# Kernel optimization log

Measured on AMD Instinct MI355X. Metric: run time of the kernel, lower is better.

## Reference

```python
import jax, jax.numpy as jnp
import numpy as np

N, E = 50000, 800000
IN_DIM, HID, OUT = 128, 64, 64
NEG_SLOPE = 0.2  # PyG GATConv default leaky_relu slope


def glorot(key, shape):
    fan_in, fan_out = shape[0], shape[-1]
    lim = jnp.sqrt(6.0 / (fan_in + fan_out))
    return jax.random.uniform(key, shape, minval=-lim, maxval=lim, dtype=jnp.float32)


def setup_inputs() -> dict:
    key = jax.random.key(0)
    ks = jax.random.split(key, 10)
    x = jax.random.normal(ks[0], (N, IN_DIM), dtype=jnp.float32)
    edge_index = jax.random.randint(ks[1], (2, E), 0, N, dtype=jnp.int64)
    # GATConv layer 1: heads=2, concat=False
    W1 = glorot(ks[2], (IN_DIM, 2 * HID))
    att_src1 = glorot(ks[3], (1, 2, HID))[0]   # [2, HID]
    att_dst1 = glorot(ks[4], (1, 2, HID))[0]
    b1 = jnp.zeros((HID,), jnp.float32)
    # GATConv layer 2: heads=1, concat=False
    W2 = glorot(ks[5], (HID, OUT))
    att_src2 = glorot(ks[6], (1, 1, OUT))[0]   # [1, OUT]
    att_dst2 = glorot(ks[7], (1, 1, OUT))[0]
    b2 = jnp.zeros((OUT,), jnp.float32)
    return {"x": x, "edge_index": edge_index, "W1": W1, "att_src1": att_src1,
            "att_dst1": att_dst1, "b1": b1, "W2": W2, "att_src2": att_src2,
            "att_dst2": att_dst2, "b2": b2}


def gat_conv(x, src, dst, W, att_src, att_dst, bias, heads, out_ch):
    n = x.shape[0]
    h = (x @ W).reshape(n, heads, out_ch)              # [N,H,C]
    a_src = jnp.einsum('nhc,hc->nh', h, att_src)       # [N,H]
    a_dst = jnp.einsum('nhc,hc->nh', h, att_dst)
    e = jax.nn.leaky_relu(a_src[src] + a_dst[dst], NEG_SLOPE)  # [E,H]
    # softmax over incoming edges per destination node (stable)
    e_max = jax.ops.segment_max(e, dst, num_segments=n)
    ex = jnp.exp(e - e_max[dst])
    denom = jax.ops.segment_sum(ex, dst, num_segments=n)
    alpha = ex / (denom[dst] + 1e-16)                  # [E,H]
    msg = h[src] * alpha[:, :, None]                   # [E,H,C]
    out = jax.ops.segment_sum(msg, dst, num_segments=n)
    return out.mean(axis=1) + bias                     # concat=False -> head mean


def reference(x, edge_index, W1, att_src1, att_dst1, b1, W2, att_src2, att_dst2, b2):
    n = x.shape[0]
    loop = jnp.arange(n, dtype=edge_index.dtype)
    src = jnp.concatenate([edge_index[0], loop])       # PyG add_self_loops
    dst = jnp.concatenate([edge_index[1], loop])
    x1 = gat_conv(x, src, dst, W1, att_src1, att_dst1, b1, 2, HID)
    x1 = jax.nn.elu(x1)
    # eval mode: dropedge and dropout are identity
    out = gat_conv(x1, src, dst, W2, att_src2, att_dst2, b2, 1, OUT)
    return out
```

## Files before the change

### kernel.cpp

```cpp
#include <hip/hip_runtime.h>
#include <math.h>

#define IN_DIM 128
#define HID 64
#define NEG_SLOPE 0.2f
#define CHUNK 4096
#define GCAP 6144

typedef __attribute__((ext_vector_type(8))) short bf16x8;
typedef __attribute__((ext_vector_type(4))) float f32x4;
typedef __attribute__((ext_vector_type(2))) float v2f;

__device__ __forceinline__ float wmax(float v){
  #pragma unroll
  for (int o = 32; o > 0; o >>= 1) v = fmaxf(v, __shfl_xor(v, o));
  return v;
}
__device__ __forceinline__ float wsum(float v){
  #pragma unroll
  for (int o = 32; o > 0; o >>= 1) v += __shfl_xor(v, o);
  return v;
}
__device__ __forceinline__ unsigned short f2bf(float f){
  union { float f; unsigned u; } v; v.f = f;
  unsigned r = v.u + 0x7fffu + ((v.u >> 16) & 1u);
  return (unsigned short)(r >> 16);
}
__device__ __forceinline__ float bl(unsigned u){
  union { unsigned u; float f; } v; v.u = u << 16; return v.f;
}
__device__ __forceinline__ float bh(unsigned u){
  union { unsigned u; float f; } v; v.u = u & 0xffff0000u; return v.f;
}
__device__ __forceinline__ v2f up2(unsigned u){
  v2f r; r[0] = bl(u); r[1] = bh(u); return r;
}

__device__ __forceinline__ void incl_scan256(int* sh, int tid){
  #pragma unroll
  for (int off = 1; off < 256; off <<= 1){
    int v = sh[tid];
    if (tid >= off) v += sh[tid - off];
    __syncthreads();
    sh[tid] = v;
    __syncthreads();
  }
}


__global__ __launch_bounds__(256) void pack_hist(const int* __restrict__ ei, int E,
                                                 unsigned* __restrict__ packed,
                                                 int* __restrict__ binCnt){
  __shared__ int lh[256];
  int tid = threadIdx.x;
  lh[tid] = 0; __syncthreads();
  int base = blockIdx.x * CHUNK;
  #pragma unroll
  for (int j = 0; j < CHUNK / 256; j++){
    int e = base + j * 256 + tid;
    if (e < E){
      unsigned s = (unsigned)ei[e];
      unsigned d = (unsigned)ei[E + e];
      unsigned pk = (d << 16) | s;
      packed[e] = pk;
      atomicAdd(&lh[d >> 8], 1);
    }
  }
  __syncthreads();
  if (lh[tid] > 0) atomicAdd(&binCnt[tid], lh[tid]);
}

__global__ __launch_bounds__(256) void scan_bins(const int* __restrict__ binCnt,
                                                 int* __restrict__ binBase,
                                                 int* __restrict__ binCursor,
                                                 int* __restrict__ row_ptr,
                                                 int NG, int N, int E){
  __shared__ int sh[256];
  int tid = threadIdx.x;
  sh[tid] = (tid < NG) ? binCnt[tid] : 0;
  __syncthreads();
  incl_scan256(sh, tid);
  int excl = tid ? sh[tid - 1] : 0;
  if (tid < NG){ binBase[tid] = excl; binCursor[tid] = excl; }
  if (tid == 0) row_ptr[N] = E;
}

__global__ __launch_bounds__(256) void scatter_bins(const unsigned* __restrict__ packed, int E,
                                                    int* __restrict__ binCursor,
                                                    unsigned* __restrict__ binned){
  __shared__ int lh[256], lbase[256], gpos[256], lcur[256];
  __shared__ unsigned buf[CHUNK];
  int tid = threadIdx.x;
  lh[tid] = 0; __syncthreads();
  int base = blockIdx.x * CHUNK;
  int rem = E - base;
  unsigned v[CHUNK / 256];
  #pragma unroll
  for (int j = 0; j < CHUNK / 256; j++){
    int i = j * 256 + tid;
    if (i < rem){ v[j] = packed[base + i]; atomicAdd(&lh[v[j] >> 24], 1); }
  }
  __syncthreads();
  lbase[tid] = lh[tid]; __syncthreads();
  incl_scan256(lbase, tid);
  int myExcl = tid ? lbase[tid - 1] : 0;
  __syncthreads();
  lbase[tid] = myExcl;
  lcur[tid] = myExcl;
  if (lh[tid] > 0) gpos[tid] = atomicAdd(&binCursor[tid], lh[tid]);
  __syncthreads();
  #pragma unroll
  for (int j = 0; j < CHUNK / 256; j++){
    int i = j * 256 + tid;
    if (i < rem){
      int b = v[j] >> 24;
      int p = atomicAdd(&lcur[b], 1);
      buf[p] = v[j];
    }
  }
  __syncthreads();
  int cn = rem < CHUNK ? rem : CHUNK;
  for (int i = tid; i < cn; i += 256){
    unsigned u = buf[i];
    int b = u >> 24;
    binned[gpos[b] + (i - lbase[b])] = u;
  }
}

__global__ __launch_bounds__(256) void group_sort(const unsigned* __restrict__ binned,
                                                  const int* __restrict__ binBase,
                                                  const int* __restrict__ binCnt,
                                                  unsigned* __restrict__ sorted,
                                                  int* __restrict__ row_ptr, int N){
  __shared__ unsigned A[GCAP], B[GCAP];
  __shared__ int h2[256], rs[256], cur[256];
  int g = blockIdx.x, tid = threadIdx.x;
  int base = binBase[g];
  int cnt = binCnt[g]; if (cnt > GCAP) cnt = GCAP;
  h2[tid] = 0; __syncthreads();
  for (int i = tid; i < cnt; i += 256){
    unsigned u = binned[base + i];
    A[i] = u;
    atomicAdd(&h2[(u >> 16) & 255], 1);
  }
  __syncthreads();
  rs[tid] = h2[tid]; __syncthreads();
  incl_scan256(rs, tid);
  int excl = tid ? rs[tid - 1] : 0;
  __syncthreads();
  rs[tid] = excl; cur[tid] = excl;
  int d = g * 256 + tid;
  if (d < N) row_ptr[d] = base + excl;
  __syncthreads();
  for (int i = tid; i < cnt; i += 256){
    unsigned u = A[i];
    int p = atomicAdd(&cur[(u >> 16) & 255], 1);
    B[p] = u;
  }
  __syncthreads();
  for (int i = tid; i < cnt; i += 256)
    sorted[base + i] = B[i];
}


__global__ void convert_w(const float* __restrict__ W1, const float* __restrict__ W2,
                          unsigned short* __restrict__ W1t, unsigned short* __restrict__ W2t){
  int tid = blockIdx.x * 256 + threadIdx.x;
  if (tid < 128 * 128){
    int n = tid >> 7, k = tid & 127;
    W1t[n * 128 + k] = f2bf(W1[k * 128 + n]);
  }
  int t2 = tid - 128 * 128;
  if (t2 >= 0 && t2 < 64 * 64){
    int n = t2 >> 6, k = t2 & 63;
    W2t[n * 64 + k] = f2bf(W2[k * 64 + n]);
  }
}

template<int K, int NC, int HEADS>
__global__ __launch_bounds__(512) void gemm_mfma(const float* __restrict__ X,
    const unsigned short* __restrict__ Wt, const float* __restrict__ asrc,
    const float* __restrict__ adst, unsigned short* __restrict__ Hb,
    float* __restrict__ aa, int n_rows)
{
  constexpr int MT = 128;
  constexpr int KP = K + 8;
  constexpr int CP = NC + 4;
  constexpr int MF = MT / 16;
  constexpr int NFt = NC / 16;
  constexpr int WPN = 8 / NFt;
  constexpr int MFW = MF / WPN;
  constexpr unsigned SM1 = (unsigned)(MT + NC) * KP * 2;
  constexpr unsigned SM2 = (unsigned)MT * CP * 4;
  __shared__ char smem[SM1 > SM2 ? SM1 : SM2];
  unsigned short* xa = (unsigned short*)smem;
  unsigned short* wl = xa + MT * KP;
  int tid = threadIdx.x;
  int n0 = blockIdx.x * MT;

  for (int idx = tid; idx < MT * (K / 4); idx += 512){
    int n = idx / (K / 4), k4 = idx % (K / 4);
    float4 v = make_float4(0.f, 0.f, 0.f, 0.f);
    if (n0 + n < n_rows) v = *(const float4*)&X[(size_t)(n0 + n) * K + k4 * 4];
    ushort4 pk; pk.x = f2bf(v.x); pk.y = f2bf(v.y); pk.z = f2bf(v.z); pk.w = f2bf(v.w);
    *(ushort4*)&xa[n * KP + k4 * 4] = pk;
  }
  for (int idx = tid; idx < NC * (K / 8); idx += 512){
    int n = idx / (K / 8), k8 = idx % (K / 8);
    uint4 v = *(const uint4*)&Wt[(size_t)n * K + k8 * 8];
    *(uint4*)&wl[n * KP + k8 * 8] = v;
  }
  __syncthreads();

  int lane = tid & 63, w = tid >> 6;
  int m = lane & 15, q = lane >> 4;
  int nf = w % NFt;
  int mseg = w / NFt;
  f32x4 acc[MFW];
  #pragma unroll
  for (int i = 0; i < MFW; i++)
    #pragma unroll
    for (int r = 0; r < 4; r++) acc[i][r] = 0.f;

  #pragma unroll
  for (int ks = 0; ks < K / 32; ks++){
    bf16x8 bg = *(const bf16x8*)&wl[(nf * 16 + m) * KP + ks * 32 + q * 8];
    #pragma unroll
    for (int i = 0; i < MFW; i++){
      bf16x8 af = *(const bf16x8*)&xa[((mseg * MFW + i) * 16 + m) * KP + ks * 32 + q * 8];
      acc[i] = __builtin_amdgcn_mfma_f32_16x16x32_bf16(af, bg, acc[i], 0, 0, 0);
    }
  }
  __syncthreads();
  float* C = (float*)smem;
  #pragma unroll
  for (int i = 0; i < MFW; i++)
    #pragma unroll
    for (int r = 0; r < 4; r++)
      C[((mseg * MFW + i) * 16 + q * 4 + r) * CP + nf * 16 + m] = acc[i][r];
  __syncthreads();

  constexpr int CH = NC / 4;
  int row = tid >> 2;
  int c0 = (tid & 3) * CH;
  int n = n0 + row;
  int head = (HEADS == 2) ? (c0 >> 6) : 0;
  float s_p = 0.f, d_p = 0.f;
  unsigned short hb[CH];
  #pragma unroll
  for (int c = 0; c < CH; c += 4){
    f32x4 v = *(const f32x4*)&C[row * CP + c0 + c];
    #pragma unroll
    for (int u = 0; u < 4; u++){
      int ch = (c0 + c + u) & 63;
      s_p += v[u] * asrc[head * 64 + ch];
      d_p += v[u] * adst[head * 64 + ch];
      hb[c + u] = f2bf(v[u]);
    }
  }
  if (n < n_rows){
    #pragma unroll
    for (int c = 0; c < CH; c += 8){
      uint4 pk;
      pk.x = (unsigned)hb[c]     | ((unsigned)hb[c + 1] << 16);
      pk.y = (unsigned)hb[c + 2] | ((unsigned)hb[c + 3] << 16);
      pk.z = (unsigned)hb[c + 4] | ((unsigned)hb[c + 5] << 16);
      pk.w = (unsigned)hb[c + 6] | ((unsigned)hb[c + 7] << 16);
      *(uint4*)&Hb[(size_t)n * NC + c0 + c] = pk;
    }
  }
  s_p += __shfl_xor(s_p, 1);
  d_p += __shfl_xor(d_p, 1);
  if (HEADS == 2){
    if ((tid & 1) == 0 && n < n_rows){
      aa[(size_t)n * 4 + head]     = s_p;
      aa[(size_t)n * 4 + 2 + head] = d_p;
    }
  } else {
    s_p += __shfl_xor(s_p, 2);
    d_p += __shfl_xor(d_p, 2);
    if ((tid & 3) == 0 && n < n_rows){
      aa[(size_t)n * 2]     = s_p;
      aa[(size_t)n * 2 + 1] = d_p;
    }
  }
}


__global__ void agg_layer1(const int* __restrict__ row_ptr, const unsigned* __restrict__ sorted,
                           const float* __restrict__ aa, const unsigned short* __restrict__ h1b,
                           const float* __restrict__ b1, float* __restrict__ x1, int n_nodes){
  int d = (blockIdx.x * blockDim.x + threadIdx.x) >> 6;
  int lane = threadIdx.x & 63;
  if (d >= n_nodes) return;
  int rp0 = row_ptr[d];
  int deg = row_ptr[d + 1] - rp0;
  float2 adv = *(const float2*)&aa[d * 4 + 2];
  int s = -1;
  if (lane < deg) s = (int)(sorted[rp0 + lane] & 0xffffu);
  else if (lane == deg) s = d;
  float e0 = -INFINITY, e1 = -INFINITY;
  if (s >= 0){
    float2 asv = *(const float2*)&aa[s * 4];
    float t0 = asv.x + adv.x;
    float t1 = asv.y + adv.y;
    e0 = t0 >= 0.f ? t0 : NEG_SLOPE * t0;
    e1 = t1 >= 0.f ? t1 : NEG_SLOPE * t1;
  }
  float m0 = wmax(e0), m1 = wmax(e1);
  float p0 = (s >= 0) ? __expf(e0 - m0) : 0.f;
  float p1 = (s >= 0) ? __expf(e1 - m1) : 0.f;
  float al0 = p0 / (wsum(p0) + 1e-16f);
  float al1 = p1 / (wsum(p1) + 1e-16f);
  int ne = deg + 1;
  int g = lane >> 4, c = lane & 15;
  v2f acc[4] = {{0.f,0.f},{0.f,0.f},{0.f,0.f},{0.f,0.f}};
  #pragma unroll 2
  for (int j0 = 0; j0 < ne; j0 += 4){
    int j = j0 + g;
    int sj = __shfl(s, j);
    float a0 = __shfl(al0, j);
    float a1 = __shfl(al1, j);
    if (j < ne){
      uint4 v = ((const uint4*)(h1b + (size_t)sj * 128))[c];
      float a = (c < 8) ? a0 : a1;
      v2f av = {a, a};
      acc[0] = av * up2(v.x) + acc[0];
      acc[1] = av * up2(v.y) + acc[1];
      acc[2] = av * up2(v.z) + acc[2];
      acc[3] = av * up2(v.w) + acc[3];
    }
  }
  float accf[8] = {acc[0][0], acc[0][1], acc[1][0], acc[1][1],
                   acc[2][0], acc[2][1], acc[3][0], acc[3][1]};
  #pragma unroll
  for (int i = 0; i < 8; i++){
    accf[i] += __shfl_xor(accf[i], 16);
    accf[i] += __shfl_xor(accf[i], 32);
  }
  float outv[8];
  #pragma unroll
  for (int i = 0; i < 8; i++){
    float o = __shfl_xor(accf[i], 8);
    outv[i] = 0.5f * (accf[i] + o);
  }
  if (g == 0 && c < 8){
    float r[8];
    #pragma unroll
    for (int i = 0; i < 8; i++){
      float v = outv[i] + b1[c * 8 + i];
      r[i] = v > 0.f ? v : expm1f(v);
    }
    float* p = &x1[(size_t)d * 64 + c * 8];
    *(float4*)p       = make_float4(r[0], r[1], r[2], r[3]);
    *(float4*)(p + 4) = make_float4(r[4], r[5], r[6], r[7]);
  }
}

__global__ void agg_layer2(const int* __restrict__ row_ptr, const unsigned* __restrict__ sorted,
                           const float* __restrict__ aa, const unsigned short* __restrict__ h2b,
                           const float* __restrict__ b2, float* __restrict__ out, int n_nodes){
  int d = (blockIdx.x * blockDim.x + threadIdx.x) >> 6;
  int lane = threadIdx.x & 63;
  if (d >= n_nodes) return;
  int rp0 = row_ptr[d];
  int deg = row_ptr[d + 1] - rp0;
  float ad = aa[d * 2 + 1];
  int s = -1;
  if (lane < deg) s = (int)(sorted[rp0 + lane] & 0xffffu);
  else if (lane == deg) s = d;
  float e = -INFINITY;
  if (s >= 0){
    float t = aa[s * 2 + 0] + ad;
    e = t >= 0.f ? t : NEG_SLOPE * t;
  }
  float m = wmax(e);
  float p = (s >= 0) ? __expf(e - m) : 0.f;
  float al = p / (wsum(p) + 1e-16f);
  int ne = deg + 1;
  int g = lane >> 3, c = lane & 7;
  v2f acc[4] = {{0.f,0.f},{0.f,0.f},{0.f,0.f},{0.f,0.f}};
  #pragma unroll 2
  for (int j0 = 0; j0 < ne; j0 += 8){
    int j = j0 + g;
    int sj = __shfl(s, j);
    float a = __shfl(al, j);
    if (j < ne){
      uint4 v = ((const uint4*)(h2b + (size_t)sj * 64))[c];
      v2f av = {a, a};
      acc[0] = av * up2(v.x) + acc[0];
      acc[1] = av * up2(v.y) + acc[1];
      acc[2] = av * up2(v.z) + acc[2];
      acc[3] = av * up2(v.w) + acc[3];
    }
  }
  float accf[8] = {acc[0][0], acc[0][1], acc[1][0], acc[1][1],
                   acc[2][0], acc[2][1], acc[3][0], acc[3][1]};
  #pragma unroll
  for (int i = 0; i < 8; i++){
    accf[i] += __shfl_xor(accf[i], 8);
    accf[i] += __shfl_xor(accf[i], 16);
    accf[i] += __shfl_xor(accf[i], 32);
  }
  if (lane < 8){
    float r[8];
    #pragma unroll
    for (int i = 0; i < 8; i++) r[i] = accf[i] + b2[lane * 8 + i];
    float* q = &out[(size_t)d * 64 + lane * 8];
    *(float4*)q       = make_float4(r[0], r[1], r[2], r[3]);
    *(float4*)(q + 4) = make_float4(r[4], r[5], r[6], r[7]);
  }
}

extern "C" void kernel_launch(void* const* d_in, const int* in_sizes, int n_in,
                              void* d_out, int out_size, void* d_ws, size_t ws_size,
                              hipStream_t stream){
  const float* x     = (const float*)d_in[0];
  const int*   ei    = (const int*)d_in[1];
  const float* W1    = (const float*)d_in[2];
  const float* asrc1 = (const float*)d_in[3];
  const float* adst1 = (const float*)d_in[4];
  const float* b1    = (const float*)d_in[5];
  const float* W2    = (const float*)d_in[6];
  const float* asrc2 = (const float*)d_in[7];
  const float* adst2 = (const float*)d_in[8];
  const float* b2    = (const float*)d_in[9];
  float* out = (float*)d_out;
  int N = in_sizes[0] / IN_DIM;
  int E = in_sizes[1] / 2;
  int NG = (N + 255) >> 8;
  int NBLK = (E + CHUNK - 1) / CHUNK;

  char* p = (char*)d_ws;
  unsigned short* h1b = (unsigned short*)p;  p += (size_t)N * 128 * 2;
  unsigned short* h2b = (unsigned short*)p;  p += (size_t)N * 64 * 2;
  float* x1  = (float*)p;                    p += (size_t)N * 64 * 4;
  float* aa1 = (float*)p;                    p += (size_t)N * 4 * 4;
  float* aa2 = (float*)p;                    p += (size_t)N * 2 * 4;
  unsigned* packed = (unsigned*)p;           p += (size_t)E * 4;
  unsigned* binned = (unsigned*)p;           p += (size_t)E * 4;
  unsigned* sorted = (unsigned*)p;           p += (size_t)E * 4;
  int* row_ptr   = (int*)p;                  p += (size_t)(N + 1) * 4;
  int* binCnt    = (int*)p;                  p += 256 * 4;
  int* binBase   = (int*)p;                  p += 256 * 4;
  int* binCursor = (int*)p;                  p += 256 * 4;
  unsigned short* W1t = (unsigned short*)p;  p += 128 * 128 * 2;
  unsigned short* W2t = (unsigned short*)p;

  hipMemsetAsync(binCnt, 0, 256 * sizeof(int), stream);
  convert_w<<<(128 * 128 + 64 * 64 + 255) / 256, 256, 0, stream>>>(W1, W2, W1t, W2t);
  pack_hist<<<NBLK, 256, 0, stream>>>(ei, E, packed, binCnt);
  scan_bins<<<1, 256, 0, stream>>>(binCnt, binBase, binCursor, row_ptr, NG, N, E);
  scatter_bins<<<NBLK, 256, 0, stream>>>(packed, E, binCursor, binned);
  group_sort<<<NG, 256, 0, stream>>>(binned, binBase, binCnt, sorted, row_ptr, N);
  gemm_mfma<128, 128, 2><<<(N + 127) / 128, 512, 0, stream>>>(
      x, W1t, asrc1, adst1, h1b, aa1, N);
  agg_layer1<<<(N + 3) / 4, 256, 0, stream>>>(row_ptr, sorted, aa1, h1b, b1, x1, N);
  gemm_mfma<64, 64, 1><<<(N + 127) / 128, 512, 0, stream>>>(
      x1, W2t, asrc2, adst2, h2b, aa2, N);
  agg_layer2<<<(N + 3) / 4, 256, 0, stream>>>(row_ptr, sorted, aa2, h2b, b2, out, N);
}
```

Baseline: 237.3 us.

## Slice hidden features per XCD and precompute attention weights before aggregation

The GEMM epilogue now writes the bf16 hidden features in a channel-sliced layout: four 16-word slices for layer 1 and two for layer 2. Attention softmax coefficients are computed in separate kernels and stored per edge, reusing dead workspace buffers. The aggregation kernels interleave block indices so that each XCD in the round-robin dispatch always gathers the same feature slice. This is meant to let each slice's gather working set fit in a per-XCD L2. The cost is narrower 4-byte gathers, with edge indices and alphas re-read once per slice, plus two extra launches.

```diff
diff --git a/kernel.cpp b/kernel.cpp
--- a/kernel.cpp
+++ b/kernel.cpp
@@ -180,8 +180,8 @@
 template<int K, int NC, int HEADS>
 __global__ __launch_bounds__(512) void gemm_mfma(const float* __restrict__ X,
     const unsigned short* __restrict__ Wt, const float* __restrict__ asrc,
-    const float* __restrict__ adst, unsigned short* __restrict__ Hb,
-    float* __restrict__ aa, int n_rows)
+    const float* __restrict__ adst, unsigned* __restrict__ Hs,
+    float* __restrict__ aa, int n_rows, int Nn)
 {
   constexpr int MT = 128;
   constexpr int KP = K + 8;
@@ -240,56 +240,65 @@
       C[((mseg * MFW + i) * 16 + q * 4 + r) * CP + nf * 16 + m] = acc[i][r];
   __syncthreads();
 
-  constexpr int CH = NC / 4;
   int row = tid >> 2;
-  int c0 = (tid & 3) * CH;
   int n = n0 + row;
-  int head = (HEADS == 2) ? (c0 >> 6) : 0;
-  float s_p = 0.f, d_p = 0.f;
-  unsigned short hb[CH];
-  #pragma unroll
-  for (int c = 0; c < CH; c += 4){
-    f32x4 v = *(const f32x4*)&C[row * CP + c0 + c];
+  if (HEADS == 2){
+    int sl = tid & 3;
+    float s0 = 0.f, s1 = 0.f, d0 = 0.f, d1 = 0.f;
+    unsigned pk[16];
     #pragma unroll
-    for (int u = 0; u < 4; u++){
-      int ch = (c0 + c + u) & 63;
-      s_p += v[u] * asrc[head * 64 + ch];
-      d_p += v[u] * adst[head * 64 + ch];
-      hb[c + u] = f2bf(v[u]);
-    }
-  }
-  if (n < n_rows){
+    for (int c = 0; c < 16; c++){
+      int ch = sl * 16 + c;
+      float v0 = C[row * CP + ch];
+      float v1 = C[row * CP + 64 + ch];
+      s0 += v0 * asrc[ch];      d0 += v0 * adst[ch];
+      s1 += v1 * asrc[64 + ch]; d1 += v1 * adst[64 + ch];
+      pk[c] = (unsigned)f2bf(v0) | ((unsigned)f2bf(v1) << 16);
+    }
+    if (n < n_rows){
+      uint4* dst = (uint4*)&Hs[((size_t)sl * Nn + n) * 16];
+      #pragma unroll
+      for (int q4 = 0; q4 < 4; q4++)
+        dst[q4] = make_uint4(pk[q4*4], pk[q4*4+1], pk[q4*4+2], pk[q4*4+3]);
+    }
+    s0 += __shfl_xor(s0, 1); s1 += __shfl_xor(s1, 1);
+    d0 += __shfl_xor(d0, 1); d1 += __shfl_xor(d1, 1);
+    s0 += __shfl_xor(s0, 2); s1 += __shfl_xor(s1, 2);
+    d0 += __shfl_xor(d0, 2); d1 += __shfl_xor(d1, 2);
+    if (sl == 0 && n < n_rows)
+      *(float4*)&aa[(size_t)n * 4] = make_float4(s0, s1, d0, d1);
+  } else {
+    int qt = tid & 3;
+    int sl = qt >> 1, half = qt & 1;
+    float sp = 0.f, dp = 0.f;
+    unsigned pk[8];
     #pragma unroll
-    for (int c = 0; c < CH; c += 8){
-      uint4 pk;
-      pk.x = (unsigned)hb[c]     | ((unsigned)hb[c + 1] << 16);
-      pk.y = (unsigned)hb[c + 2] | ((unsigned)hb[c + 3] << 16);
-      pk.z = (unsigned)hb[c + 4] | ((unsigned)hb[c + 5] << 16);
-      pk.w = (unsigned)hb[c + 6] | ((unsigned)hb[c + 7] << 16);
-      *(uint4*)&Hb[(size_t)n * NC + c0 + c] = pk;
-    }
-  }
-  s_p += __shfl_xor(s_p, 1);
-  d_p += __shfl_xor(d_p, 1);
-  if (HEADS == 2){
-    if ((tid & 1) == 0 && n < n_rows){
-      aa[(size_t)n * 4 + head]     = s_p;
-      aa[(size_t)n * 4 + 2 + head] = d_p;
-    }
-  } else {
-    s_p += __shfl_xor(s_p, 2);
-    d_p += __shfl_xor(d_p, 2);
-    if ((tid & 3) == 0 && n < n_rows){
-      aa[(size_t)n * 2]     = s_p;
-      aa[(size_t)n * 2 + 1] = d_p;
-    }
-  }
-}
-
-
-__global__ void agg_layer1(const int* __restrict__ row_ptr, const unsigned* __restrict__ sorted,
-                           const float* __restrict__ aa, const unsigned short* __restrict__ h1b,
-                           const float* __restrict__ b1, float* __restrict__ x1, int n_nodes){
+    for (int c2 = 0; c2 < 8; c2++){
+      int ch = qt * 16 + c2 * 2;
+      float v0 = C[row * CP + ch];
+      float v1 = C[row * CP + ch + 1];
+      sp += v0 * asrc[ch] + v1 * asrc[ch + 1];
+      dp += v0 * adst[ch] + v1 * adst[ch + 1];
+      pk[c2] = (unsigned)f2bf(v0) | ((unsigned)f2bf(v1) << 16);
+    }
+    if (n < n_rows){
+      uint4* dst = (uint4*)&Hs[((size_t)sl * Nn + n) * 16 + half * 8];
+      dst[0] = make_uint4(pk[0], pk[1], pk[2], pk[3]);
+      dst[1] = make_uint4(pk[4], pk[5], pk[6], pk[7]);
+    }
+    sp += __shfl_xor(sp, 1); dp += __shfl_xor(dp, 1);
+    sp += __shfl_xor(sp, 2); dp += __shfl_xor(dp, 2);
+    if (qt == 0 && n < n_rows){
+      aa[(size_t)n * 2]     = sp;
+      aa[(size_t)n * 2 + 1] = dp;
+    }
+  }
+}
+
+
+__global__ void alpha1_k(const int* __restrict__ row_ptr, const unsigned* __restrict__ sorted,
+                         const float* __restrict__ aa, float2* __restrict__ alpha,
+                         float2* __restrict__ aself, int n_nodes){
   int d = (blockIdx.x * blockDim.x + threadIdx.x) >> 6;
   int lane = threadIdx.x & 63;
   if (d >= n_nodes) return;
@@ -312,54 +321,13 @@
   float p1 = (s >= 0) ? __expf(e1 - m1) : 0.f;
   float al0 = p0 / (wsum(p0) + 1e-16f);
   float al1 = p1 / (wsum(p1) + 1e-16f);
-  int ne = deg + 1;
-  int g = lane >> 4, c = lane & 15;
-  v2f acc[4] = {{0.f,0.f},{0.f,0.f},{0.f,0.f},{0.f,0.f}};
-  #pragma unroll 2
-  for (int j0 = 0; j0 < ne; j0 += 4){
-    int j = j0 + g;
-    int sj = __shfl(s, j);
-    float a0 = __shfl(al0, j);
-    float a1 = __shfl(al1, j);
-    if (j < ne){
-      uint4 v = ((const uint4*)(h1b + (size_t)sj * 128))[c];
-      float a = (c < 8) ? a0 : a1;
-      v2f av = {a, a};
-      acc[0] = av * up2(v.x) + acc[0];
-      acc[1] = av * up2(v.y) + acc[1];
-      acc[2] = av * up2(v.z) + acc[2];
-      acc[3] = av * up2(v.w) + acc[3];
-    }
-  }
-  float accf[8] = {acc[0][0], acc[0][1], acc[1][0], acc[1][1],
-                   acc[2][0], acc[2][1], acc[3][0], acc[3][1]};
-  #pragma unroll
-  for (int i = 0; i < 8; i++){
-    accf[i] += __shfl_xor(accf[i], 16);
-    accf[i] += __shfl_xor(accf[i], 32);
-  }
-  float outv[8];
-  #pragma unroll
-  for (int i = 0; i < 8; i++){
-    float o = __shfl_xor(accf[i], 8);
-    outv[i] = 0.5f * (accf[i] + o);
-  }
-  if (g == 0 && c < 8){
-    float r[8];
-    #pragma unroll
-    for (int i = 0; i < 8; i++){
-      float v = outv[i] + b1[c * 8 + i];
-      r[i] = v > 0.f ? v : expm1f(v);
-    }
-    float* p = &x1[(size_t)d * 64 + c * 8];
-    *(float4*)p       = make_float4(r[0], r[1], r[2], r[3]);
-    *(float4*)(p + 4) = make_float4(r[4], r[5], r[6], r[7]);
-  }
-}
-
-__global__ void agg_layer2(const int* __restrict__ row_ptr, const unsigned* __restrict__ sorted,
-                           const float* __restrict__ aa, const unsigned short* __restrict__ h2b,
-                           const float* __restrict__ b2, float* __restrict__ out, int n_nodes){
+  if (lane < deg)       alpha[rp0 + lane] = make_float2(al0, al1);
+  else if (lane == deg) aself[d]          = make_float2(al0, al1);
+}
+
+__global__ void alpha2_k(const int* __restrict__ row_ptr, const unsigned* __restrict__ sorted,
+                         const float* __restrict__ aa, float* __restrict__ alpha,
+                         float* __restrict__ aself, int n_nodes){
   int d = (blockIdx.x * blockDim.x + threadIdx.x) >> 6;
   int lane = threadIdx.x & 63;
   if (d >= n_nodes) return;
@@ -377,38 +345,93 @@
   float m = wmax(e);
   float p = (s >= 0) ? __expf(e - m) : 0.f;
   float al = p / (wsum(p) + 1e-16f);
+  if (lane < deg)       alpha[rp0 + lane] = al;
+  else if (lane == deg) aself[d]          = al;
+}
+
+__global__ __launch_bounds__(256) void agg1s(const int* __restrict__ row_ptr,
+    const unsigned* __restrict__ sorted, const float2* __restrict__ alpha,
+    const float2* __restrict__ aself, const unsigned* __restrict__ h1s,
+    const float* __restrict__ b1, float* __restrict__ x1, int Nn){
+  int b = blockIdx.x;
+  int j8 = b & 7;
+  int slice = j8 >> 1;
+  int dg = ((b >> 3) << 1) + (j8 & 1);
+  int d = dg * 4 + (threadIdx.x >> 6);
+  if (d >= Nn) return;
+  int lane = threadIdx.x & 63;
+  int rp0 = row_ptr[d];
+  int deg = row_ptr[d + 1] - rp0;
   int ne = deg + 1;
-  int g = lane >> 3, c = lane & 7;
-  v2f acc[4] = {{0.f,0.f},{0.f,0.f},{0.f,0.f},{0.f,0.f}};
+  int g = lane >> 4, c = lane & 15;
+  const unsigned* hbase = h1s + (size_t)slice * Nn * 16 + c;
+  v2f acc = {0.f, 0.f};
   #pragma unroll 2
-  for (int j0 = 0; j0 < ne; j0 += 8){
+  for (int j0 = 0; j0 < ne; j0 += 4){
     int j = j0 + g;
-    int sj = __shfl(s, j);
-    float a = __shfl(al, j);
-    if (j < ne){
-      uint4 v = ((const uint4*)(h2b + (size_t)sj * 64))[c];
-      v2f av = {a, a};
-      acc[0] = av * up2(v.x) + acc[0];
-      acc[1] = av * up2(v.y) + acc[1];
-      acc[2] = av * up2(v.z) + acc[2];
-      acc[3] = av * up2(v.w) + acc[3];
-    }
-  }
-  float accf[8] = {acc[0][0], acc[0][1], acc[1][0], acc[1][1],
-                   acc[2][0], acc[2][1], acc[3][0], acc[3][1]};
-  #pragma unroll
-  for (int i = 0; i < 8; i++){
-    accf[i] += __shfl_xor(accf[i], 8);
-    accf[i] += __shfl_xor(accf[i], 16);
-    accf[i] += __shfl_xor(accf[i], 32);
-  }
-  if (lane < 8){
-    float r[8];
-    #pragma unroll
-    for (int i = 0; i < 8; i++) r[i] = accf[i] + b2[lane * 8 + i];
-    float* q = &out[(size_t)d * 64 + lane * 8];
-    *(float4*)q       = make_float4(r[0], r[1], r[2], r[3]);
-    *(float4*)(q + 4) = make_float4(r[4], r[5], r[6], r[7]);
+    int sj; v2f av;
+    if (j < deg){
+      sj = (int)(sorted[rp0 + j] & 0xffffu);
+      float2 t = alpha[rp0 + j]; av[0] = t.x; av[1] = t.y;
+    } else if (j == deg){
+      sj = d;
+      float2 t = aself[d]; av[0] = t.x; av[1] = t.y;
+    } else {
+      sj = d; av[0] = 0.f; av[1] = 0.f;
+    }
+    unsigned hv = hbase[(size_t)sj * 16];
+    acc = av * up2(hv) + acc;
+  }
+  acc[0] += __shfl_xor(acc[0], 16); acc[1] += __shfl_xor(acc[1], 16);
+  acc[0] += __shfl_xor(acc[0], 32); acc[1] += __shfl_xor(acc[1], 32);
+  if (g == 0){
+    int ch = slice * 16 + c;
+    float v = 0.5f * (acc[0] + acc[1]) + b1[ch];
+    x1[(size_t)d * 64 + ch] = v > 0.f ? v : expm1f(v);
+  }
+}
+
+__global__ __launch_bounds__(256) void agg2s(const int* __restrict__ row_ptr,
+    const unsigned* __restrict__ sorted, const float* __restrict__ alpha,
+    const float* __restrict__ aself, const unsigned* __restrict__ h2s,
+    const float* __restrict__ b2, float* __restrict__ out, int Nn){
+  int b = blockIdx.x;
+  int j8 = b & 7;
+  int slice = j8 >> 2;
+  int dg = ((b >> 3) << 2) + (j8 & 3);
+  int d = dg * 4 + (threadIdx.x >> 6);
+  if (d >= Nn) return;
+  int lane = threadIdx.x & 63;
+  int rp0 = row_ptr[d];
+  int deg = row_ptr[d + 1] - rp0;
+  int ne = deg + 1;
+  int g = lane >> 4, c = lane & 15;
+  const unsigned* hbase = h2s + (size_t)slice * Nn * 16 + c;
+  v2f acc = {0.f, 0.f};
+  #pragma unroll 2
+  for (int j0 = 0; j0 < ne; j0 += 4){
+    int j = j0 + g;
+    int sj; float a;
+    if (j < deg){
+      sj = (int)(sorted[rp0 + j] & 0xffffu);
+      a = alpha[rp0 + j];
+    } else if (j == deg){
+      sj = d; a = aself[d];
+    } else {
+      sj = d; a = 0.f;
+    }
+    unsigned hv = hbase[(size_t)sj * 16];
+    v2f av = {a, a};
+    acc = av * up2(hv) + acc;
+  }
+  acc[0] += __shfl_xor(acc[0], 16); acc[1] += __shfl_xor(acc[1], 16);
+  acc[0] += __shfl_xor(acc[0], 32); acc[1] += __shfl_xor(acc[1], 32);
+  if (g == 0){
+    int ch = slice * 32 + c * 2;
+    float2 r;
+    r.x = acc[0] + b2[ch];
+    r.y = acc[1] + b2[ch + 1];
+    *(float2*)&out[(size_t)d * 64 + ch] = r;
   }
 }
 
@@ -430,10 +453,11 @@
   int E = in_sizes[1] / 2;
   int NG = (N + 255) >> 8;
   int NBLK = (E + CHUNK - 1) / CHUNK;
+  int ngrp = (N + 3) / 4;
 
   char* p = (char*)d_ws;
-  unsigned short* h1b = (unsigned short*)p;  p += (size_t)N * 128 * 2;
-  unsigned short* h2b = (unsigned short*)p;  p += (size_t)N * 64 * 2;
+  unsigned* h1s = (unsigned*)p;              p += (size_t)N * 64 * 4;
+  unsigned* h2s = (unsigned*)p;              p += (size_t)N * 32 * 4;
   float* x1  = (float*)p;                    p += (size_t)N * 64 * 4;
   float* aa1 = (float*)p;                    p += (size_t)N * 4 * 4;
   float* aa2 = (float*)p;                    p += (size_t)N * 2 * 4;
@@ -444,8 +468,12 @@
   int* binCnt    = (int*)p;                  p += 256 * 4;
   int* binBase   = (int*)p;                  p += 256 * 4;
   int* binCursor = (int*)p;                  p += 256 * 4;
+  float2* aself1 = (float2*)p;               p += (size_t)N * 8;
+  float*  aself2 = (float*)p;                p += (size_t)N * 4;
   unsigned short* W1t = (unsigned short*)p;  p += 128 * 128 * 2;
   unsigned short* W2t = (unsigned short*)p;
+  float2* alpha1 = (float2*)packed;
+  float*  alpha2 = (float*)x1;
 
   hipMemsetAsync(binCnt, 0, 256 * sizeof(int), stream);
   convert_w<<<(128 * 128 + 64 * 64 + 255) / 256, 256, 0, stream>>>(W1, W2, W1t, W2t);
@@ -454,9 +482,13 @@
   scatter_bins<<<NBLK, 256, 0, stream>>>(packed, E, binCursor, binned);
   group_sort<<<NG, 256, 0, stream>>>(binned, binBase, binCnt, sorted, row_ptr, N);
   gemm_mfma<128, 128, 2><<<(N + 127) / 128, 512, 0, stream>>>(
-      x, W1t, asrc1, adst1, h1b, aa1, N);
-  agg_layer1<<<(N + 3) / 4, 256, 0, stream>>>(row_ptr, sorted, aa1, h1b, b1, x1, N);
+      x, W1t, asrc1, adst1, h1s, aa1, N, N);
+  alpha1_k<<<ngrp, 256, 0, stream>>>(row_ptr, sorted, aa1, alpha1, aself1, N);
+  agg1s<<<((ngrp + 1) / 2) * 8, 256, 0, stream>>>(
+      row_ptr, sorted, alpha1, aself1, h1s, b1, x1, N);
   gemm_mfma<64, 64, 1><<<(N + 127) / 128, 512, 0, stream>>>(
-      x1, W2t, asrc2, adst2, h2b, aa2, N);
-  agg_layer2<<<(N + 3) / 4, 256, 0, stream>>>(row_ptr, sorted, aa2, h2b, b2, out, N);
-}
+      x1, W2t, asrc2, adst2, h2s, aa2, N, N);
+  alpha2_k<<<ngrp, 256, 0, stream>>>(row_ptr, sorted, aa2, alpha2, aself2, N);
+  agg2s<<<((ngrp + 3) / 4) * 8, 256, 0, stream>>>(
+      row_ptr, sorted, alpha2, aself2, h2s, b2, out, N);
+}
```

After: 335.4 us. 1.41x slower.
